# Optimization experiments

Hardware: AMD Instinct MI355X
Metric: run time of the kernel (lower is better)

The kernel has to match this reference:

```python
import jax, jax.numpy as jnp
import numpy as np

B, N, D = 2, 2048, 1024
H, QH, DH = 8, 16, 64        # kv heads, query heads, head dim
SOFTCLAMP = 50.0


def setup_inputs() -> dict:
    key = jax.random.key(0)
    ks = jax.random.split(key, 7)
    return {
        "tokens": jax.random.normal(ks[0], (B, N, D), jnp.float32),
        "norm_w": jnp.ones((D,), jnp.float32) + 0.02 * jax.random.normal(ks[1], (D,), jnp.float32),
        "Wq":  0.02 * jax.random.normal(ks[2], (D, QH * DH), jnp.float32),
        "Wkv": 0.02 * jax.random.normal(ks[3], (D, 2 * H * DH), jnp.float32),
        "Wout": 0.02 * jax.random.normal(ks[4], (H * DH, D), jnp.float32),
        "q_gamma": 0.02 * jax.random.normal(ks[5], (QH, DH), jnp.float32),
        "k_gamma": 0.02 * jax.random.normal(ks[6], (H, DH), jnp.float32),
    }


def _rmsnorm(x, w):
    eps = jnp.finfo(x.dtype).eps
    return x * jax.lax.rsqrt(jnp.mean(x * x, axis=-1, keepdims=True) + eps) * w


def _l2norm(x):
    # F.normalize(dim=-1, p=2) clamps the norm at eps=1e-12
    n = jnp.maximum(jnp.linalg.norm(x, axis=-1, keepdims=True), 1e-12)
    return x / n


def _mh_rmsnorm(x, gamma):
    # x: [b, h, n, d]; gamma: [h, d]; scale = (gamma + 1) * sqrt(d)
    scale = (gamma + 1.0) * np.sqrt(x.shape[-1]).astype(np.float32)
    return _l2norm(x) * scale[None, :, None, :]


def reference(tokens, norm_w, Wq, Wkv, Wout, q_gamma, k_gamma):
    b, n, d = tokens.shape
    x = _rmsnorm(tokens, norm_w)

    q = (x @ Wq).reshape(b, n, QH, DH).transpose(0, 2, 1, 3)      # [b, QH, n, dh]
    kv = x @ Wkv
    k = kv[..., : H * DH].reshape(b, n, H, DH).transpose(0, 2, 1, 3)  # [b, H, n, dh]
    v = kv[..., H * DH:].reshape(b, n, H, DH).transpose(0, 2, 1, 3)   # [b, H, n, dh]

    q = _mh_rmsnorm(q, q_gamma)
    k = _mh_rmsnorm(k, k_gamma)

    g = QH // H
    q = q.reshape(b, H, g, n, DH)                                 # [b, h, g, i, dh]

    sim = jnp.einsum('bhgid,bhjd->bhgij', q, k)                   # [b, h, g, i, j]
    sim = jnp.tanh(sim / SOFTCLAMP) * SOFTCLAMP                   # softcap BEFORE scale (faithful)
    sim = sim * (DH ** -0.5)

    neg = -jnp.finfo(sim.dtype).max
    causal = jnp.triu(jnp.ones((n, n), dtype=bool), 1)
    sim = jnp.where(causal, neg, sim)

    attn = jax.nn.softmax(sim, axis=-1)
    # NOTE: original einsum sums over the group axis g -> [b, h, i, dh]
    out = jnp.einsum('bhgij,bhjd->bhid', attn, v)
    out = out.transpose(0, 2, 1, 3).reshape(b, n, H * DH)
    return out @ Wout
```

## Files before the change

### kernel.cpp

```cpp
#include <hip/hip_runtime.h>
#include <hip/hip_bf16.h>
#include <type_traits>

typedef unsigned short u16;
typedef __attribute__((ext_vector_type(2))) float f32x2;
typedef __attribute__((ext_vector_type(4))) float f32x4;
typedef __attribute__((ext_vector_type(8))) short short8;
typedef __attribute__((ext_vector_type(4))) short short4v;
typedef __attribute__((ext_vector_type(8))) __bf16 bf16x8;
typedef __attribute__((ext_vector_type(4))) __bf16 bf16x4;

#define BB 2
#define NN 2048
#define DDIM 1024
#define HH 8
#define QHH 16
#define DHH 64

__device__ __forceinline__ float b2f(u16 v) {
    return __builtin_bit_cast(float, ((unsigned)v) << 16);
}
__device__ __forceinline__ u16 f2b(float f) {
    unsigned u = __builtin_bit_cast(unsigned, f);
    u += 0x7FFFu + ((u >> 16) & 1u);
    return (u16)(u >> 16);
}
__device__ __forceinline__ float fastrcp(float x) {
#if __has_builtin(__builtin_amdgcn_rcpf)
    return __builtin_amdgcn_rcpf(x);
#else
    return 1.0f / x;
#endif
}
__device__ __forceinline__ float fastexp2(float x) {
#if __has_builtin(__builtin_amdgcn_exp2f)
    return __builtin_amdgcn_exp2f(x);
#else
    return exp2f(x);
#endif
}
__device__ __forceinline__ f32x2 sp2(float v) { return (f32x2){v, v}; }
__device__ __forceinline__ f32x4 mfma16(short8 a, short8 b, f32x4 c) {
    return __builtin_amdgcn_mfma_f32_16x16x32_bf16(
        __builtin_bit_cast(bf16x8, a), __builtin_bit_cast(bf16x8, b), c, 0, 0, 0);
}
#if __has_builtin(__builtin_amdgcn_mfma_f32_16x16x16_bf16)
__device__ __forceinline__ f32x4 mfma_k16(short4v a, short4v b, f32x4 c) {
    return __builtin_amdgcn_mfma_f32_16x16x16_bf16(
        __builtin_bit_cast(bf16x4, a), __builtin_bit_cast(bf16x4, b), c, 0, 0, 0);
}
#else
__device__ __forceinline__ f32x4 mfma_k16(short4v a, short4v b, f32x4 c) {
    return __builtin_amdgcn_mfma_f32_16x16x16bf16_1k(a, b, c, 0, 0, 0);
}
#endif
__device__ __forceinline__ void stage16(const u16* g, u16* l, int lane) {
#if __has_builtin(__builtin_amdgcn_global_load_lds)
    __builtin_amdgcn_global_load_lds(
        (const __attribute__((address_space(1))) unsigned int*)g,
        (__attribute__((address_space(3))) unsigned int*)l, 16, 0, 0);
#else
    *(short8*)(l + lane * 8) = *(const short8*)g;
#endif
}

__global__ __launch_bounds__(256) void k_rmsnorm(const float* __restrict__ tokens,
                                                 const float* __restrict__ norm_w,
                                                 u16* __restrict__ xb) {
    const int row = blockIdx.x;
    const int tid = threadIdx.x;
    const float* xp = tokens + (size_t)row * DDIM + tid * 4;
    float4 raw = *(const float4*)xp;
    float ss = raw.x * raw.x + raw.y * raw.y + raw.z * raw.z + raw.w * raw.w;
#pragma unroll
    for (int d = 1; d < 64; d <<= 1) ss += __shfl_xor(ss, d);
    __shared__ float red[4];
    if ((tid & 63) == 0) red[tid >> 6] = ss;
    __syncthreads();
    float tot = red[0] + red[1] + red[2] + red[3];
    float r = rsqrtf(tot * (1.0f / 1024.0f) + 1.1920929e-7f);
    float4 wv = *(const float4*)(norm_w + tid * 4);
    ushort4 o;
    o.x = f2b(raw.x * r * wv.x);
    o.y = f2b(raw.y * r * wv.y);
    o.z = f2b(raw.z * r * wv.z);
    o.w = f2b(raw.w * r * wv.w);
    *(ushort4*)(xb + (size_t)row * DDIM + tid * 4) = o;
}

__global__ __launch_bounds__(256) void k_wprep(const float* __restrict__ Wq,
                                               const float* __restrict__ Wkv,
                                               const float* __restrict__ Wout,
                                               u16* __restrict__ WqT,
                                               u16* __restrict__ WkvT,
                                               u16* __restrict__ WoutT) {
    const int z = blockIdx.z;
    const float* in = (z == 0) ? Wq : (z == 1) ? Wkv : Wout;
    u16* out = (z == 0) ? WqT : (z == 1) ? WkvT : WoutT;
    const int R = (z == 2) ? 512 : 1024, C = 1024;
    const int br = blockIdx.y * 32;
    if (br >= R) return;
    __shared__ u16 tile[32][33];
    const int bc = blockIdx.x * 32;
    const int tx = threadIdx.x & 31, ty = threadIdx.x >> 5;
#pragma unroll
    for (int i = 0; i < 32; i += 8) tile[ty + i][tx] = f2b(in[(size_t)(br + ty + i) * C + bc + tx]);
    __syncthreads();
#pragma unroll
    for (int i = 0; i < 32; i += 8) out[(size_t)(bc + ty + i) * R + br + tx] = tile[tx][ty + i];
}

__global__ __launch_bounds__(256) void k_gemm128(const u16* __restrict__ A,
                                                 const u16* __restrict__ Bt,
                                                 u16* __restrict__ C,
                                                 int M, int Ncols, int K) {
    __shared__ __attribute__((aligned(16))) u16 As[128 * 32];
    __shared__ __attribute__((aligned(16))) u16 Bs[128 * 32];
    const int tid = threadIdx.x;
    const int lane = tid & 63;
    const int w = tid >> 6;
    const int m0 = blockIdx.y * 128;
    const int n0 = blockIdx.x * 128;
    const int wr = (w >> 1) * 64;
    const int wc = (w & 1) * 64;
    const int lr = lane & 15;
    const int lq = lane >> 4;

    const int ch0 = w * 32;
    const u16* aSrc = A + (size_t)(m0 + ch0 + (lane >> 2)) * K + (lane & 3) * 8;
    const u16* bSrc = Bt + (size_t)(n0 + ch0 + (lane >> 2)) * K + (lane & 3) * 8;
    u16* aDst = As + ch0 * 32;
    u16* bDst = Bs + ch0 * 32;

    f32x4 acc[4][4];
#pragma unroll
    for (int i = 0; i < 4; i++)
#pragma unroll
        for (int j = 0; j < 4; j++) acc[i][j] = (f32x4){0.f, 0.f, 0.f, 0.f};

    for (int k0 = 0; k0 < K; k0 += 32) {
        __syncthreads();
        stage16(aSrc, aDst, lane);
        stage16(aSrc + (size_t)16 * K, aDst + 512, lane);
        stage16(bSrc, bDst, lane);
        stage16(bSrc + (size_t)16 * K, bDst + 512, lane);
        aSrc += 32;
        bSrc += 32;
        __syncthreads();
        short8 a[4], b[4];
#pragma unroll
        for (int mi = 0; mi < 4; ++mi) a[mi] = *(const short8*)&As[(wr + mi * 16 + lr) * 32 + lq * 8];
#pragma unroll
        for (int ni = 0; ni < 4; ++ni) b[ni] = *(const short8*)&Bs[(wc + ni * 16 + lr) * 32 + lq * 8];
#pragma unroll
        for (int mi = 0; mi < 4; ++mi)
#pragma unroll
            for (int ni = 0; ni < 4; ++ni) acc[mi][ni] = mfma16(a[mi], b[ni], acc[mi][ni]);
    }
#pragma unroll
    for (int mi = 0; mi < 4; ++mi)
#pragma unroll
        for (int ni = 0; ni < 4; ++ni)
#pragma unroll
            for (int r = 0; r < 4; ++r) {
                int row = m0 + wr + mi * 16 + lq * 4 + r;
                int col = n0 + wc + ni * 16 + lr;
                C[(size_t)row * Ncols + col] = f2b(acc[mi][ni][r]);
            }
}

__global__ __launch_bounds__(256) void k_gemm64f(const u16* __restrict__ A,
                                                 const u16* __restrict__ Bt,
                                                 float* __restrict__ C,
                                                 int M, int Ncols, int K) {
    __shared__ __attribute__((aligned(16))) u16 As[64 * 32];
    __shared__ __attribute__((aligned(16))) u16 Bs[128 * 32];
    const int tid = threadIdx.x;
    const int lane = tid & 63;
    const int w = tid >> 6;
    const int m0 = blockIdx.y * 64;
    const int n0 = blockIdx.x * 128;
    const int lr = lane & 15;
    const int lq = lane >> 4;

    const u16* aSrc = A + (size_t)(m0 + w * 16 + (lane >> 2)) * K + (lane & 3) * 8;
    const u16* bSrc = Bt + (size_t)(n0 + w * 32 + (lane >> 2)) * K + (lane & 3) * 8;
    u16* aDst = As + w * 16 * 32;
    u16* bDst = Bs + w * 32 * 32;

    f32x4 acc[8];
#pragma unroll
    for (int i = 0; i < 8; i++) acc[i] = (f32x4){0.f, 0.f, 0.f, 0.f};

    for (int k0 = 0; k0 < K; k0 += 32) {
        __syncthreads();
        stage16(aSrc, aDst, lane);
        stage16(bSrc, bDst, lane);
        stage16(bSrc + (size_t)16 * K, bDst + 512, lane);
        aSrc += 32;
        bSrc += 32;
        __syncthreads();
        short8 a = *(const short8*)&As[(w * 16 + lr) * 32 + lq * 8];
#pragma unroll
        for (int nt = 0; nt < 8; ++nt) {
            short8 b = *(const short8*)&Bs[(nt * 16 + lr) * 32 + lq * 8];
            acc[nt] = mfma16(a, b, acc[nt]);
        }
    }
#pragma unroll
    for (int nt = 0; nt < 8; ++nt)
#pragma unroll
        for (int r = 0; r < 4; ++r) {
            int row = m0 + w * 16 + lq * 4 + r;
            int col = n0 + nt * 16 + lr;
            C[(size_t)row * Ncols + col] = acc[nt][r];
        }
}

__global__ __launch_bounds__(256) void k_headnorm(const u16* __restrict__ qkv,
                                                  const float* __restrict__ q_gamma,
                                                  const float* __restrict__ k_gamma,
                                                  u16* __restrict__ qn,
                                                  u16* __restrict__ kn) {
    const int row = blockIdx.x;
    const int b = row >> 11, n = row & 2047;
    const int lane = threadIdx.x & 63, w = threadIdx.x >> 6;
    const u16* qr = qkv + (size_t)row * 2048;
    const u16* kvr = qkv + (size_t)row * 2048 + 1024;
#pragma unroll
    for (int t = 0; t < 4; ++t) {
        int qh = w * 4 + t;
        float v = b2f(qr[qh * 64 + lane]);
        float ss = v * v;
#pragma unroll
        for (int d = 1; d < 64; d <<= 1) ss += __shfl_xor(ss, d);
        float nrm = fmaxf(sqrtf(ss), 1e-12f);
        float g = q_gamma[qh * 64 + lane];
        qn[((size_t)(b * QHH + qh) * NN + n) * 64 + lane] = f2b(v / nrm * (g + 1.0f) * 8.0f);
    }
#pragma unroll
    for (int t = 0; t < 2; ++t) {
        int kh = w * 2 + t;
        float v = b2f(kvr[kh * 64 + lane]);
        float ss = v * v;
#pragma unroll
        for (int d = 1; d < 64; d <<= 1) ss += __shfl_xor(ss, d);
        float nrm = fmaxf(sqrtf(ss), 1e-12f);
        float g = k_gamma[kh * 64 + lane];
        kn[((size_t)(b * HH + kh) * NN + n) * 64 + lane] = f2b(v / nrm * (g + 1.0f) * 0.16f);
    }
}

__global__ __launch_bounds__(256) void k_vtrans(const u16* __restrict__ qkv,
                                                u16* __restrict__ vt) {
    const int bh = blockIdx.x;
    const int b = bh >> 3, h = bh & 7;
    const int n0 = blockIdx.y * 64;
    const int tid = threadIdx.x;
    __shared__ u16 t[64 * 72];
#pragma unroll
    for (int it = 0; it < 2; ++it) {
        int idx = tid + it * 256;
        int i = idx >> 3, c = idx & 7;
        short8 v = *(const short8*)&qkv[(size_t)(b * NN + n0 + i) * 2048 + 1536 + h * 64 + c * 8];
        *(short8*)&t[i * 72 + c * 8] = v;
    }
    __syncthreads();
#pragma unroll
    for (int it = 0; it < 2; ++it) {
        int idx = tid + it * 256;
        int d = idx >> 3, c = idx & 7;
        const int sw = (d >> 3) & 1;
        u16 tmp[8], o[8];
#pragma unroll
        for (int j = 0; j < 8; ++j) tmp[j] = t[(c * 8 + j) * 72 + d];
#pragma unroll
        for (int j = 0; j < 8; ++j) o[j] = tmp[j ^ (sw << 2)];
        *(short8*)&vt[((size_t)(bh * 64 + d)) * NN + n0 + c * 8] = *(short8*)o;
    }
}

__global__ __launch_bounds__(256) void k_attn(const u16* __restrict__ qn,
                                              const u16* __restrict__ kn,
                                              const u16* __restrict__ vt,
                                              u16* __restrict__ OT) {
    const int bq = blockIdx.x;
    const int b = bq >> 4, qh = bq & 15;
    const int h = qh >> 1;
    const int tid = threadIdx.x;
    const int lane = tid & 63, w = tid >> 6;
    const int lr = lane & 15, lq = lane >> 4;
    const int z = 31 - blockIdx.y;
    const int i0 = z * 64 + w * 16;
    const int ntile = z + 1;
    const int irow = i0 + lr;

    const u16* Qp = qn + (size_t)(b * QHH + qh) * NN * 64;
    const u16* Kp = kn + (size_t)(b * HH + h) * NN * 64;
    const u16* Vp = vt + (size_t)(b * HH + h) * 64 * NN;
    u16* Op = OT + (size_t)(b * QHH + qh) * NN * 64;

    __shared__ __attribute__((aligned(16))) u16 Ks[2][64 * 64];
    __shared__ __attribute__((aligned(16))) u16 Vs[2][64 * 64];

    short8 qf0 = *(const short8*)&Qp[(size_t)(i0 + lr) * 64 + lq * 8];
    short8 qf1 = *(const short8*)&Qp[(size_t)(i0 + lr) * 64 + 32 + lq * 8];

    f32x4 of[4];
#pragma unroll
    for (int dt = 0; dt < 4; ++dt) of[dt] = (f32x4){0.f, 0.f, 0.f, 0.f};
    f32x2 ls = {0.f, 0.f};

    const int srow = lane >> 3;
    const int sch = (lane ^ srow) & 7;
    const int rA = w * 16, rB = w * 16 + 8;

    const u16* kSrcA = Kp + (size_t)(rA + srow) * 64 + sch * 8;
    const u16* kSrcB = Kp + (size_t)(rB + srow) * 64 + sch * 8;
    const u16* vSrcA = Vp + (size_t)(rA + srow) * NN + sch * 8;
    const u16* vSrcB = Vp + (size_t)(rB + srow) * NN + sch * 8;

    auto stageKV = [&](int buf) {
        stage16(kSrcA, &Ks[buf][rA * 64], lane);
        stage16(kSrcB, &Ks[buf][rB * 64], lane);
        stage16(vSrcA, &Vs[buf][rA * 64], lane);
        stage16(vSrcB, &Vs[buf][rB * 64], lane);
        kSrcA += 64 * 64;
        kSrcB += 64 * 64;
        vSrcA += 64;
        vSrcB += 64;
    };

    auto smax = [&](f32x4 sc, int lim, bool masked) -> short4v {
        f32x2 xa = {sc[0], sc[1]};
        f32x2 xb = {sc[2], sc[3]};
        f32x2 ya = xa * xa;
        f32x2 yb = xb * xb;
        f32x2 Ga = __builtin_elementwise_fma(ya, __builtin_elementwise_fma(ya,
                       __builtin_elementwise_fma(ya, __builtin_elementwise_fma(ya,
                           sp2(0.04705711f), sp2(-0.32327190f)), sp2(1.11500760f)),
                       sp2(-2.98719110f)), sp2(9.01599730f));
        f32x2 Gb = __builtin_elementwise_fma(yb, __builtin_elementwise_fma(yb,
                       __builtin_elementwise_fma(yb, __builtin_elementwise_fma(yb,
                           sp2(0.04705711f), sp2(-0.32327190f)), sp2(1.11500760f)),
                       sp2(-2.98719110f)), sp2(9.01599730f));
        f32x2 aa = __builtin_elementwise_fma(xa, Ga, sp2(-9.0168440f));
        f32x2 ab = __builtin_elementwise_fma(xb, Gb, sp2(-9.0168440f));
        float p0 = fastexp2(aa.x);
        float p1 = fastexp2(aa.y);
        float p2 = fastexp2(ab.x);
        float p3 = fastexp2(ab.y);
        if (masked) {
            p0 = (0 <= lim) ? p0 : 0.0f;
            p1 = (1 <= lim) ? p1 : 0.0f;
            p2 = (2 <= lim) ? p2 : 0.0f;
            p3 = (3 <= lim) ? p3 : 0.0f;
        }
        ls += (f32x2){p0, p1};
        ls += (f32x2){p2, p3};
        bf16x4 pb;
        pb[0] = (__bf16)p0;
        pb[1] = (__bf16)p1;
        pb[2] = (__bf16)p2;
        pb[3] = (__bf16)p3;
        return __builtin_bit_cast(short4v, pb);
    };

    auto tile = [&](int buf, int jt) {
        const int j0 = jt << 6;
        const u16* kb = &Ks[buf][0];
        const u16* vb = &Vs[buf][0];
        f32x4 sc[4];
        __builtin_amdgcn_s_setprio(1);
#pragma unroll
        for (int ct = 0; ct < 4; ++ct) {
            const int r = ct * 16 + lr;
            short8 kf0 = *(const short8*)&kb[r * 64 + ((lq ^ (lr & 7)) << 3)];
            short8 kf1 = *(const short8*)&kb[r * 64 + (((4 + lq) ^ (lr & 7)) << 3)];
            f32x4 t = (f32x4){0.f, 0.f, 0.f, 0.f};
            t = mfma16(kf0, qf0, t);
            t = mfma16(kf1, qf1, t);
            sc[ct] = t;
        }
        __builtin_amdgcn_s_setprio(0);
        const bool masked = (jt == ntile - 1);
        short4v pk[4];
#pragma unroll
        for (int ct = 0; ct < 4; ++ct) {
            const int lim = irow - (j0 + ct * 16 + lq * 4);
            pk[ct] = smax(sc[ct], lim, masked);
        }
        __builtin_amdgcn_s_setprio(1);
#pragma unroll
        for (int dt = 0; dt < 4; ++dt) {
            const int d = dt * 16 + lr;
#pragma unroll
            for (int ct = 0; ct < 4; ++ct) {
                short4v vf = *(const short4v*)
                    &vb[d * 64 + ((((ct << 1) + (lq >> 1)) ^ (lr & 7)) << 3) +
                        (((lq ^ (lr >> 3)) & 1) << 2)];
                of[dt] = mfma_k16(vf, pk[ct], of[dt]);
            }
        }
        __builtin_amdgcn_s_setprio(0);
    };

    stageKV(0);
    for (int jt = 0; jt < ntile; ++jt) {
        const int buf = jt & 1;
        __syncthreads();
        if (jt + 1 < ntile) stageKV(buf ^ 1);
        tile(buf, jt);
    }

    float l = ls.x + ls.y;
    l += __shfl_xor(l, 16);
    l += __shfl_xor(l, 32);
    const float inv = fastrcp(l);
#pragma unroll
    for (int dt = 0; dt < 4; ++dt) {
        u16 o[4];
#pragma unroll
        for (int r = 0; r < 4; ++r) o[r] = f2b(of[dt][r] * inv);
        *(ushort4*)&Op[(size_t)irow * 64 + dt * 16 + lq * 4] = *(ushort4*)o;
    }
}

__global__ __launch_bounds__(256) void k_gsum(const u16* __restrict__ O, u16* __restrict__ AO) {
    const int idx = blockIdx.x * 256 + threadIdx.x;
    const int c8 = idx & 63;
    const int n = (idx >> 6) & 2047;
    const int b = idx >> 17;
    const int hh = c8 >> 3;
    const u16* p0 = O + (((size_t)(b * QHH + 2 * hh) * NN) + n) * 64 + (c8 & 7) * 8;
    const u16* p1 = O + (((size_t)(b * QHH + 2 * hh + 1) * NN) + n) * 64 + (c8 & 7) * 8;
    short8 a = *(const short8*)p0;
    short8 c = *(const short8*)p1;
    u16 o[8];
#pragma unroll
    for (int j = 0; j < 8; ++j)
        o[j] = f2b(b2f((u16)a[j]) + b2f((u16)c[j]));
    *(short8*)&AO[((size_t)(b * NN + n)) * 512 + c8 * 8] = *(short8*)o;
}

extern "C" void kernel_launch(void* const* d_in, const int* in_sizes, int n_in,
                              void* d_out, int out_size, void* d_ws, size_t ws_size,
                              hipStream_t stream) {
    const float* tokens = (const float*)d_in[0];
    const float* norm_w = (const float*)d_in[1];
    const float* Wq = (const float*)d_in[2];
    const float* Wkv = (const float*)d_in[3];
    const float* Wout = (const float*)d_in[4];
    const float* q_gamma = (const float*)d_in[5];
    const float* k_gamma = (const float*)d_in[6];
    float* out = (float*)d_out;

    char* ws = (char*)d_ws;
    u16* xb = (u16*)(ws + 0);
    u16* WqT = (u16*)(ws + 8388608);
    u16* WkvT = (u16*)(ws + 10485760);
    u16* WoutT = (u16*)(ws + 12582912);
    u16* qkv = (u16*)(ws + 13631488);
    u16* kn = (u16*)(ws + 30408704);
    u16* vtb = (u16*)(ws + 34603008);
    u16* qn = xb;
    u16* Obuf = qkv;
    u16* AO = (u16*)(ws + 22020096);

    k_rmsnorm<<<4096, 256, 0, stream>>>(tokens, norm_w, xb);
    k_wprep<<<dim3(32, 32, 3), 256, 0, stream>>>(Wq, Wkv, Wout, WqT, WkvT, WoutT);
    k_gemm128<<<dim3(16, 32), 256, 0, stream>>>(xb, WqT, qkv, 4096, 2048, 1024);
    k_headnorm<<<4096, 256, 0, stream>>>(qkv, q_gamma, k_gamma, qn, kn);
    k_vtrans<<<dim3(16, 32), 256, 0, stream>>>(qkv, vtb);
    k_attn<<<dim3(32, 32), 256, 0, stream>>>(qn, kn, vtb, Obuf);
    k_gsum<<<1024, 256, 0, stream>>>(Obuf, AO);
    k_gemm64f<<<dim3(8, 64), 256, 0, stream>>>(AO, WoutT, out, 4096, 1024, 512);
}
```

Before: 186.0 us.

## Split attention KV range across two blocks and combine partials in gsum

Each attention block now handles half of the causal key range for a query tile, doubling the grid. Unnormalized partial outputs and row sums are written to workspace, and the group-sum kernel merges the two halves and normalizes. This is a split-K approach meant to balance the causal triangle's uneven work and raise occupancy. The cost is extra global traffic for partial outputs and a wider combine step. Because the softmax uses a fixed max from the softcap bound rather than a running max, no rescaling is needed. Partials are stored in bf16 before normalization, which may lose some precision.

```diff
diff --git a/kernel.cpp b/kernel.cpp
--- a/kernel.cpp
+++ b/kernel.cpp
@@ -283,22 +283,30 @@
 __global__ __launch_bounds__(256) void k_attn(const u16* __restrict__ qn,
                                               const u16* __restrict__ kn,
                                               const u16* __restrict__ vt,
-                                              u16* __restrict__ OT) {
+                                              u16* __restrict__ OT,
+                                              float* __restrict__ Lp) {
     const int bq = blockIdx.x;
     const int b = bq >> 4, qh = bq & 15;
     const int h = qh >> 1;
     const int tid = threadIdx.x;
     const int lane = tid & 63, w = tid >> 6;
     const int lr = lane & 15, lq = lane >> 4;
-    const int z = 31 - blockIdx.y;
+    const int y = blockIdx.y;
+    const int z = 31 - (y >> 1);
+    const int s = y & 1;
+    const int ntile = z + 1;
+    const int jmid = (ntile + 1) >> 1;
+    const int jb = s ? jmid : 0;
+    const int je = s ? ntile : jmid;
+    const int ntl = je - jb;
     const int i0 = z * 64 + w * 16;
-    const int ntile = z + 1;
     const int irow = i0 + lr;
 
     const u16* Qp = qn + (size_t)(b * QHH + qh) * NN * 64;
     const u16* Kp = kn + (size_t)(b * HH + h) * NN * 64;
     const u16* Vp = vt + (size_t)(b * HH + h) * 64 * NN;
-    u16* Op = OT + (size_t)(b * QHH + qh) * NN * 64;
+    u16* Op = OT + (size_t)s * (BB * QHH * NN * 64) + (size_t)bq * NN * 64;
+    float* Lsel = Lp + (size_t)s * (BB * QHH * NN) + (size_t)bq * NN;
 
     __shared__ __attribute__((aligned(16))) u16 Ks[2][64 * 64];
     __shared__ __attribute__((aligned(16))) u16 Vs[2][64 * 64];
@@ -315,10 +323,10 @@
     const int sch = (lane ^ srow) & 7;
     const int rA = w * 16, rB = w * 16 + 8;
 
-    const u16* kSrcA = Kp + (size_t)(rA + srow) * 64 + sch * 8;
-    const u16* kSrcB = Kp + (size_t)(rB + srow) * 64 + sch * 8;
-    const u16* vSrcA = Vp + (size_t)(rA + srow) * NN + sch * 8;
-    const u16* vSrcB = Vp + (size_t)(rB + srow) * NN + sch * 8;
+    const u16* kSrcA = Kp + (size_t)jb * 4096 + (size_t)(rA + srow) * 64 + sch * 8;
+    const u16* kSrcB = Kp + (size_t)jb * 4096 + (size_t)(rB + srow) * 64 + sch * 8;
+    const u16* vSrcA = Vp + (size_t)(rA + srow) * NN + jb * 64 + sch * 8;
+    const u16* vSrcB = Vp + (size_t)(rB + srow) * NN + jb * 64 + sch * 8;
 
     auto stageKV = [&](int buf) {
         stage16(kSrcA, &Ks[buf][rA * 64], lane);
@@ -405,41 +413,58 @@
         __builtin_amdgcn_s_setprio(0);
     };
 
-    stageKV(0);
-    for (int jt = 0; jt < ntile; ++jt) {
-        const int buf = jt & 1;
-        __syncthreads();
-        if (jt + 1 < ntile) stageKV(buf ^ 1);
-        tile(buf, jt);
+    if (ntl > 0) {
+        stageKV(0);
+        for (int t = 0; t < ntl; ++t) {
+            const int buf = t & 1;
+            __syncthreads();
+            if (t + 1 < ntl) stageKV(buf ^ 1);
+            tile(buf, jb + t);
+        }
     }
 
     float l = ls.x + ls.y;
     l += __shfl_xor(l, 16);
     l += __shfl_xor(l, 32);
-    const float inv = fastrcp(l);
 #pragma unroll
     for (int dt = 0; dt < 4; ++dt) {
         u16 o[4];
 #pragma unroll
-        for (int r = 0; r < 4; ++r) o[r] = f2b(of[dt][r] * inv);
+        for (int r = 0; r < 4; ++r) o[r] = f2b(of[dt][r]);
         *(ushort4*)&Op[(size_t)irow * 64 + dt * 16 + lq * 4] = *(ushort4*)o;
     }
-}
-
-__global__ __launch_bounds__(256) void k_gsum(const u16* __restrict__ O, u16* __restrict__ AO) {
+    if (lq == 0) Lsel[irow] = l;
+}
+
+__global__ __launch_bounds__(256) void k_gsum(const u16* __restrict__ O,
+                                              const float* __restrict__ Lp,
+                                              u16* __restrict__ AO) {
     const int idx = blockIdx.x * 256 + threadIdx.x;
     const int c8 = idx & 63;
     const int n = (idx >> 6) & 2047;
     const int b = idx >> 17;
     const int hh = c8 >> 3;
-    const u16* p0 = O + (((size_t)(b * QHH + 2 * hh) * NN) + n) * 64 + (c8 & 7) * 8;
-    const u16* p1 = O + (((size_t)(b * QHH + 2 * hh + 1) * NN) + n) * 64 + (c8 & 7) * 8;
-    short8 a = *(const short8*)p0;
-    short8 c = *(const short8*)p1;
+    const int ch = c8 & 7;
+    const int q0 = b * QHH + 2 * hh, q1 = q0 + 1;
+    const size_t SOFF = (size_t)BB * QHH * NN * 64;
+    const size_t LOFF = (size_t)BB * QHH * NN;
+    const u16* a0 = O + ((size_t)q0 * NN + n) * 64 + ch * 8;
+    const u16* a1 = O + ((size_t)q1 * NN + n) * 64 + ch * 8;
+    const u16* b0 = a0 + SOFF;
+    const u16* b1 = a1 + SOFF;
+    const float l0 = Lp[(size_t)q0 * NN + n] + Lp[LOFF + (size_t)q0 * NN + n];
+    const float l1 = Lp[(size_t)q1 * NN + n] + Lp[LOFF + (size_t)q1 * NN + n];
+    const float inv0 = fastrcp(l0);
+    const float inv1 = fastrcp(l1);
+    short8 va0 = *(const short8*)a0;
+    short8 vb0 = *(const short8*)b0;
+    short8 va1 = *(const short8*)a1;
+    short8 vb1 = *(const short8*)b1;
     u16 o[8];
 #pragma unroll
     for (int j = 0; j < 8; ++j)
-        o[j] = f2b(b2f((u16)a[j]) + b2f((u16)c[j]));
+        o[j] = f2b((b2f((u16)va0[j]) + b2f((u16)vb0[j])) * inv0 +
+                   (b2f((u16)va1[j]) + b2f((u16)vb1[j])) * inv1);
     *(short8*)&AO[((size_t)(b * NN + n)) * 512 + c8 * 8] = *(short8*)o;
 }
 
@@ -464,15 +489,16 @@
     u16* kn = (u16*)(ws + 30408704);
     u16* vtb = (u16*)(ws + 34603008);
     u16* qn = xb;
-    u16* Obuf = qkv;
-    u16* AO = (u16*)(ws + 22020096);
+    u16* Opart = qkv;
+    float* Lpart = (float*)(ws + 8388608);
+    u16* AO = kn;
 
     k_rmsnorm<<<4096, 256, 0, stream>>>(tokens, norm_w, xb);
     k_wprep<<<dim3(32, 32, 3), 256, 0, stream>>>(Wq, Wkv, Wout, WqT, WkvT, WoutT);
     k_gemm128<<<dim3(16, 32), 256, 0, stream>>>(xb, WqT, qkv, 4096, 2048, 1024);
     k_headnorm<<<4096, 256, 0, stream>>>(qkv, q_gamma, k_gamma, qn, kn);
     k_vtrans<<<dim3(16, 32), 256, 0, stream>>>(qkv, vtb);
-    k_attn<<<dim3(32, 32), 256, 0, stream>>>(qn, kn, vtb, Obuf);
-    k_gsum<<<1024, 256, 0, stream>>>(Obuf, AO);
+    k_attn<<<dim3(32, 64), 256, 0, stream>>>(qn, kn, vtb, Opart, Lpart);
+    k_gsum<<<1024, 256, 0, stream>>>(Opart, Lpart, AO);
     k_gemm64f<<<dim3(8, 64), 256, 0, stream>>>(AO, WoutT, out, 4096, 1024, 512);
 }
```

Measured after the change: 186.9 us. Within noise of the previous version (+0.5%).
